# Optimization experiments

Hardware: AMD Instinct MI355X
Metric: run time of the kernel (lower is better)

The kernel has to match this reference:

```python
import jax, jax.numpy as jnp
import numpy as np

OUT, IN, SPEC = 4096, 4096, 512


def _boundprop(last_uA, weight, bias, preact_lb, preact_ub, alpha):
    # simplex_coefficient: relu(W + b[:,None]) - relu(b[:,None]), shape [OUT, IN]
    simplex_coeff = jax.nn.relu(weight + bias[:, None]) - jax.nn.relu(bias[:, None])
    pos_uA = jnp.maximum(last_uA, 0.0)  # [1, SPEC, OUT]
    neg_uA = jnpum if False else jnp.minimum(last_uA, 0.0)

    # ---- simplex branch ----
    lb_u = preact_lb[..., None]  # [1, OUT, 1]
    ub_u = preact_ub[..., None]
    upper_coeff = jnp.where(ub_u <= 0, 0.0, jnp.where(lb_u >= 0, weight, simplex_coeff))  # [1,OUT,IN]
    upper_bias = jnp.where(preact_ub <= 0, 0.0,
                           jnp.where(preact_lb >= 0, bias, jnp.maximum(bias, 0.0)))  # [1,OUT]
    lower_d = (jnp.abs(preact_lb) >= jnp.abs(preact_ub)).astype(last_uA.dtype)  # [1,OUT]
    lower_coeff = jnp.where(ub_u <= 0, 0.0,
                            jnp.where(lb_u >= 0, weight, lower_d[..., None] * weight))  # [1,OUT,IN]
    lower_bias = jnp.where(preact_ub <= 0, 0.0,
                           jnp.where(preact_lb >= 0, bias, lower_d * bias))  # [1,OUT]
    one_minus_a = 1.0 - alpha              # [1,OUT,1]
    one_minus_a_s = 1.0 - alpha[..., 0]    # [1,OUT]
    upper_coeff = one_minus_a * upper_coeff
    lower_coeff = one_minus_a * lower_coeff
    upper_bias = one_minus_a_s * upper_bias
    lower_bias = one_minus_a_s * lower_bias
    simplex_uA = (jnp.einsum('bso,boi->bsi', pos_uA, upper_coeff)
                  + jnp.einsum('bso,boi->bsi', neg_uA, lower_coeff))  # [1,SPEC,IN]
    simplex_ubias = (jnp.einsum('bso,o->bs', pos_uA, upper_bias[0])
                     + jnp.einsum('bso,o->bs', neg_uA, lower_bias[0]))  # [1,SPEC]

    # ---- crown branch ----
    lb_r = jnp.minimum(preact_lb, 0.0)
    ub_r = jnp.maximum(preact_ub, 0.0)
    ub_r = jnp.maximum(ub_r, lb_r + 1e-8)
    upper_d = ub_r / (ub_r - lb_r)  # [1,OUT]
    upper_b = -lb_r * upper_d       # [1,OUT]
    ud = upper_d[:, None, :]        # [1,1,OUT]
    ld = (ud > 0.5).astype(last_uA.dtype)
    crown_uA_pre = ud * pos_uA + ld * neg_uA  # [1,SPEC,OUT]
    crown_ubias = jnp.einsum('bso,bo->bs', pos_uA, upper_b)  # [1,SPEC]
    w = alpha * weight              # [1,OUT,IN]
    b = alpha[..., 0] * bias        # [1,OUT]
    crown_uA = jnp.einsum('bso,boi->bsi', crown_uA_pre, w)   # [1,SPEC,IN]
    crown_ubias = crown_ubias + jnp.einsum('bso,o->bs', crown_uA_pre, b[0])

    return simplex_uA + crown_uA, simplex_ubias + crown_ubias


def setup_inputs() -> dict:
    key = jax.random.key(0)
    k1, k2, k3, k4, k5 = jax.random.split(key, 5)
    weight = jax.random.normal(k1, (OUT, IN), jnp.float32) * 0.02
    bias = jax.random.normal(k2, (OUT,), jnp.float32) * 0.02
    preact_lb = jax.random.normal(k3, (1, OUT), jnp.float32)
    # ensure ub > lb, with mixed-sign ranges so all relaxation branches are hit
    preact_ub = preact_lb + jnp.abs(jax.random.normal(k4, (1, OUT), jnp.float32)) + 1e-2
    last_uA = jax.random.normal(k5, (1, SPEC, OUT), jnp.float32)
    alpha = jnp.ones((1, OUT, 1), jnp.float32)
    return {'last_uA': last_uA, 'weight': weight, 'bias': bias,
            'preact_lb': preact_lb, 'preact_ub': preact_ub, 'alpha': alpha}


def reference(last_uA, weight, bias, preact_lb, preact_ub, alpha):
    uA, ubias = _boundprop(last_uA, weight, bias, preact_lb, preact_ub, alpha)
    return uA, ubias
```

## Files before the change

### kernel.cpp

```cpp
#include <hip/hip_runtime.h>
#include <hip/hip_bf16.h>
#include <stdint.h>

#define OUTN 4096
#define INN  4096
#define SPECN 512
#define BK 128
#define KT (OUTN / BK)

typedef __attribute__((ext_vector_type(8))) short short8;
typedef __attribute__((ext_vector_type(4))) float f32x4;

__device__ __forceinline__ ushort f2bf(float f) {
    uint32_t u = __float_as_uint(f);
    uint32_t r = (u + 0x7FFFu + ((u >> 16) & 1u)) >> 16;
    return (ushort)r;
}
__device__ __forceinline__ float bf2f(ushort u) {
    return __uint_as_float((uint32_t)u << 16);
}

__global__ __launch_bounds__(256) void prep(
    const float* __restrict__ uA, const float* __restrict__ W,
    const float* __restrict__ Bias, const float* __restrict__ Lb,
    const float* __restrict__ Ub, const float* __restrict__ Alpha,
    ushort* __restrict__ A1, ushort* __restrict__ A2, ushort* __restrict__ WT,
    unsigned long long* __restrict__ rowmask, float* __restrict__ ubias_out)
{
    const int tid = threadIdx.x;
    if (blockIdx.x < 512) {
        const int s = blockIdx.x;
        float acc = 0.f;
        unsigned long long msk = 0;
        for (int p = 0; p < 4; ++p) {
            const int o = p * 1024 + tid * 4;
            const float4 u4 = *(const float4*)&uA[(size_t)s * OUTN + o];
            const float4 lb4 = *(const float4*)&Lb[o];
            const float4 ub4 = *(const float4*)&Ub[o];
            const float4 b4 = *(const float4*)&Bias[o];
            const float4 a4 = *(const float4*)&Alpha[o];
            const float uu[4] = {u4.x, u4.y, u4.z, u4.w};
            const float lbv[4] = {lb4.x, lb4.y, lb4.z, lb4.w};
            const float ubv[4] = {ub4.x, ub4.y, ub4.z, ub4.w};
            const float bv[4] = {b4.x, b4.y, b4.z, b4.w};
            const float av[4] = {a4.x, a4.y, a4.z, a4.w};
            ushort r1[4], r2[4];
#pragma unroll
            for (int j = 0; j < 4; ++j) {
                const float u = uu[j], lb = lbv[j], ub = ubv[j], b = bv[j], a = av[j];
                const float pp = fmaxf(u, 0.f), nn = fminf(u, 0.f);
                const bool stneg = (ub <= 0.f);
                const bool stpos = (lb >= 0.f);
                const float lower_d = (fabsf(lb) >= fabsf(ub)) ? 1.f : 0.f;
                float lbr = fminf(lb, 0.f);
                float ubr = fmaxf(ub, 0.f);
                ubr = fmaxf(ubr, lbr + 1e-8f);
                const float ud = ubr / (ubr - lbr);
                const float upb = -lbr * ud;
                const float ldc = (ud > 0.5f) ? 1.f : 0.f;
                const float oma = 1.f - a;
                const float crown = ud * pp + ldc * nn;
                const float wcoef = a * crown +
                    oma * (stneg ? 0.f : (stpos ? (pp + nn) : lower_d * nn));
                const float scoef = (stneg || stpos) ? 0.f : oma * pp;
                const float ub_t = stneg ? 0.f : (stpos ? b : fmaxf(b, 0.f));
                const float lb_t = stneg ? 0.f : (stpos ? b : lower_d * b);
                acc += pp * (oma * ub_t + upb) + nn * (oma * lb_t) + crown * (a * b);
                r1[j] = f2bf(wcoef);
                r2[j] = f2bf(scoef);
            }
            *(ushort4*)&A1[(size_t)s * OUTN + o] = make_ushort4(r1[0], r1[1], r1[2], r1[3]);
            *(ushort4*)&A2[(size_t)s * OUTN + o] = make_ushort4(r2[0], r2[1], r2[2], r2[3]);
            if (((r2[0] | r2[1] | r2[2] | r2[3]) & 0x7FFF) != 0)
                msk |= 1ull << (p * 16 + (tid >> 4));
        }
#pragma unroll
        for (int off = 32; off; off >>= 1) {
            acc += __shfl_down(acc, off);
            msk |= __shfl_down(msk, off);
        }
        __shared__ float redf[4];
        __shared__ unsigned long long redm[4];
        if ((tid & 63) == 0) { redf[tid >> 6] = acc; redm[tid >> 6] = msk; }
        __syncthreads();
        if (tid == 0) {
            ubias_out[s] = redf[0] + redf[1] + redf[2] + redf[3];
            rowmask[s] = redm[0] | redm[1] | redm[2] | redm[3];
        }
    } else {
        __shared__ float t[64][65];
        const int tb = blockIdx.x - 512;
        const int bi = tb & 63, bo = tb >> 6;
        const int i0 = bi * 64, o0 = bo * 64;
        const int sub = tid >> 4;
        const int q4 = (tid & 15) * 4;
#pragma unroll
        for (int p = 0; p < 4; ++p) {
            const int ol = p * 16 + sub;
            const float4 w = *(const float4*)&W[(size_t)(o0 + ol) * INN + i0 + q4];
            t[q4 + 0][ol] = w.x;
            t[q4 + 1][ol] = w.y;
            t[q4 + 2][ol] = w.z;
            t[q4 + 3][ol] = w.w;
        }
        __syncthreads();
#pragma unroll
        for (int p = 0; p < 4; ++p) {
            const int il = p * 16 + sub;
            *(ushort4*)&WT[(size_t)(i0 + il) * OUTN + o0 + q4] =
                make_ushort4(f2bf(t[il][q4]), f2bf(t[il][q4 + 1]),
                             f2bf(t[il][q4 + 2]), f2bf(t[il][q4 + 3]));
        }
    }
}

__global__ __launch_bounds__(256) void gemm(
    const ushort* __restrict__ A1, const ushort* __restrict__ A2,
    const ushort* __restrict__ WT, const float* __restrict__ Bias,
    const unsigned long long* __restrict__ rowmask, float* __restrict__ outp)
{
    __shared__ ushort sA[2][64 * BK];
    __shared__ ushort sB[2][64 * BK];
    __shared__ unsigned long long smaskLds;

    const int bid = blockIdx.x;
    const int swz = (bid & 7) * 64 + (bid >> 3);
    const int bx = swz >> 3;
    const int by = swz & 7;
    const int i0 = bx * 64, s0 = by * 64;
    const int tid = threadIdx.x;
    const int lane = tid & 63;
    const int w = tid >> 6;
    const int wr = w >> 1, wc = w & 1;

    if (tid < 64) {
        unsigned long long v = rowmask[s0 + tid];
#pragma unroll
        for (int off = 32; off; off >>= 1) v |= __shfl_down(v, off);
        if (tid == 0) smaskLds = v;
    }

    f32x4 acc[2][2] = {};

    auto stage = [&](int buf, int t) {
        const int ko = t * BK;
#pragma unroll
        for (int h = 0; h < 4; ++h) {
            const int c = w * 4 + h;
            const int r = c * 4 + (lane >> 4);
            const int g = (lane & 15) ^ (r & 15);
            const size_t off = (size_t)ko + g * 8;
            __builtin_amdgcn_global_load_lds(
                (const __attribute__((address_space(1))) void*)(A1 + (size_t)(s0 + r) * OUTN + off),
                (__attribute__((address_space(3))) void*)&sA[buf][c * 512], 16, 0, 0);
            __builtin_amdgcn_global_load_lds(
                (const __attribute__((address_space(1))) void*)(WT + (size_t)(i0 + r) * OUTN + off),
                (__attribute__((address_space(3))) void*)&sB[buf][c * 512], 16, 0, 0);
        }
    };

    auto compute = [&](int buf) {
#pragma unroll
        for (int kk = 0; kk < BK; kk += 32) {
            short8 av[2], bv[2];
#pragma unroll
            for (int m = 0; m < 2; ++m) {
                const int r = wr * 32 + m * 16 + (lane & 15);
                const int g = ((kk >> 3) + (lane >> 4)) ^ (r & 15);
                av[m] = *(const short8*)&sA[buf][r * BK + g * 8];
            }
#pragma unroll
            for (int n = 0; n < 2; ++n) {
                const int r = wc * 32 + n * 16 + (lane & 15);
                const int g = ((kk >> 3) + (lane >> 4)) ^ (r & 15);
                bv[n] = *(const short8*)&sB[buf][r * BK + g * 8];
            }
#pragma unroll
            for (int m = 0; m < 2; ++m)
#pragma unroll
                for (int n = 0; n < 2; ++n)
                    acc[m][n] = __builtin_amdgcn_mfma_f32_16x16x32_bf16(
                        av[m], bv[n], acc[m][n], 0, 0, 0);
        }
    };

    stage(0, 0);
    __syncthreads();
    const unsigned long long smask = smaskLds;
    for (int t = 0; t < KT - 1; ++t) {
        stage((t + 1) & 1, t + 1);
        compute(t & 1);
        __syncthreads();
    }
    compute((KT - 1) & 1);

    if (smask) {
        for (int b = 0; b < 64; ++b) {
            if (!((smask >> b) & 1)) continue;
            __syncthreads();
#pragma unroll
            for (int h = 0; h < 2; ++h) {
                const int c = w * 2 + h;
                const int r = c * 8 + (lane >> 3);
                const int g = (lane & 7) ^ (r & 7);
                const size_t off = (size_t)b * 64 + g * 8;
                __builtin_amdgcn_global_load_lds(
                    (const __attribute__((address_space(1))) void*)(A2 + (size_t)(s0 + r) * OUTN + off),
                    (__attribute__((address_space(3))) void*)&sA[0][c * 512], 16, 0, 0);
                __builtin_amdgcn_global_load_lds(
                    (const __attribute__((address_space(1))) void*)(WT + (size_t)(i0 + r) * OUTN + off),
                    (__attribute__((address_space(3))) void*)&sB[0][c * 512], 16, 0, 0);
            }
            __syncthreads();
#pragma unroll
            for (int kk = 0; kk < 64; kk += 32) {
                short8 av2[2], bw[2];
#pragma unroll
                for (int m = 0; m < 2; ++m) {
                    const int r = wr * 32 + m * 16 + (lane & 15);
                    const int g = ((kk >> 3) + (lane >> 4)) ^ (r & 7);
                    av2[m] = *(const short8*)&sA[0][r * 64 + g * 8];
                }
                const int kb = kk + (lane >> 4) * 8;
                const float4 b0 = *(const float4*)&Bias[b * 64 + kb];
                const float4 b1 = *(const float4*)&Bias[b * 64 + kb + 4];
                const float bb[8] = {b0.x, b0.y, b0.z, b0.w, b1.x, b1.y, b1.z, b1.w};
#pragma unroll
                for (int n = 0; n < 2; ++n) {
                    const int r = wc * 32 + n * 16 + (lane & 15);
                    const int g = ((kk >> 3) + (lane >> 4)) ^ (r & 7);
                    const short8 wv = *(const short8*)&sB[0][r * 64 + g * 8];
                    short8 sv;
#pragma unroll
                    for (int j = 0; j < 8; ++j) {
                        const float wf = bf2f((ushort)wv[j]);
                        sv[j] = (short)f2bf(fmaxf(wf + bb[j], 0.f) - fmaxf(bb[j], 0.f));
                    }
                    bw[n] = sv;
                }
#pragma unroll
                for (int m = 0; m < 2; ++m)
#pragma unroll
                    for (int n = 0; n < 2; ++n)
                        acc[m][n] = __builtin_amdgcn_mfma_f32_16x16x32_bf16(
                            av2[m], bw[n], acc[m][n], 0, 0, 0);
            }
        }
    }

#pragma unroll
    for (int m = 0; m < 2; ++m)
#pragma unroll
        for (int n = 0; n < 2; ++n) {
            const int srow = s0 + wr * 32 + m * 16 + (lane >> 4) * 4;
            const int icol = i0 + wc * 32 + n * 16 + (lane & 15);
#pragma unroll
            for (int r = 0; r < 4; ++r)
                outp[(size_t)(srow + r) * INN + icol] = acc[m][n][r];
        }
}

extern "C" void kernel_launch(void* const* d_in, const int* in_sizes, int n_in,
                              void* d_out, int out_size, void* d_ws, size_t ws_size,
                              hipStream_t stream) {
    const float* uA    = (const float*)d_in[0];
    const float* W     = (const float*)d_in[1];
    const float* Bias  = (const float*)d_in[2];
    const float* Lb    = (const float*)d_in[3];
    const float* Ub    = (const float*)d_in[4];
    const float* Alpha = (const float*)d_in[5];
    float* outp = (float*)d_out;

    char* ws = (char*)d_ws;
    unsigned long long* rowmask = (unsigned long long*)ws;
    ushort* A1 = (ushort*)(ws + 4096);
    ushort* A2 = (ushort*)(ws + 4096 + (1u << 22));
    ushort* WT = (ushort*)(ws + 4096 + (2u << 22));

    prep<<<4608, 256, 0, stream>>>(uA, W, Bias, Lb, Ub, Alpha, A1, A2, WT,
                                   rowmask, outp + (size_t)SPECN * INN);
    gemm<<<512, 256, 0, stream>>>(A1, A2, WT, Bias, rowmask, outp);
}
```

Measured before the change: 146.6 us.

## Triple-buffer GEMM K-loop with BK 64 and a single barrier per step

Shrinks the K tile from 128 to 64 and moves from double to triple buffering in LDS. Each iteration waits on vmcnt for the older stage and then issues one raw s_barrier, so two stages of loads stay in flight while the block computes. The row-mask reduction now uses a per-wave xor shuffle instead of an LDS round-trip and the extra barrier. The tail loop reuses the stage lambda, which issues redundant A1 loads that are then overwritten by A2 loads into the same LDS slots. That adds some extra traffic and relies on the in-order completion of the two sets of writes.

```diff
diff --git a/kernel.cpp b/kernel.cpp
--- a/kernel.cpp
+++ b/kernel.cpp
@@ -5,7 +5,7 @@
 #define OUTN 4096
 #define INN  4096
 #define SPECN 512
-#define BK 128
+#define BK 64
 #define KT (OUTN / BK)
 
 typedef __attribute__((ext_vector_type(8))) short short8;
@@ -119,9 +119,8 @@
     const ushort* __restrict__ WT, const float* __restrict__ Bias,
     const unsigned long long* __restrict__ rowmask, float* __restrict__ outp)
 {
-    __shared__ ushort sA[2][64 * BK];
-    __shared__ ushort sB[2][64 * BK];
-    __shared__ unsigned long long smaskLds;
+    __shared__ ushort sA[3][64 * 64];
+    __shared__ ushort sB[3][64 * 64];
 
     const int bid = blockIdx.x;
     const int swz = (bid & 7) * 64 + (bid >> 3);
@@ -133,30 +132,30 @@
     const int w = tid >> 6;
     const int wr = w >> 1, wc = w & 1;
 
-    if (tid < 64) {
-        unsigned long long v = rowmask[s0 + tid];
-#pragma unroll
-        for (int off = 32; off; off >>= 1) v |= __shfl_down(v, off);
-        if (tid == 0) smaskLds = v;
-    }
+    unsigned long long smask = rowmask[s0 + lane];
+#pragma unroll
+    for (int off = 32; off; off >>= 1) smask |= __shfl_xor(smask, off);
 
     f32x4 acc[2][2] = {};
+
+    const int c0 = w * 2, c1 = w * 2 + 1;
+    const int rr0 = c0 * 8 + (lane >> 3), rr1 = c1 * 8 + (lane >> 3);
+    const int g0 = (lane & 7) ^ (rr0 & 7), g1 = (lane & 7) ^ (rr1 & 7);
 
     auto stage = [&](int buf, int t) {
         const int ko = t * BK;
-#pragma unroll
-        for (int h = 0; h < 4; ++h) {
-            const int c = w * 4 + h;
-            const int r = c * 4 + (lane >> 4);
-            const int g = (lane & 15) ^ (r & 15);
-            const size_t off = (size_t)ko + g * 8;
-            __builtin_amdgcn_global_load_lds(
-                (const __attribute__((address_space(1))) void*)(A1 + (size_t)(s0 + r) * OUTN + off),
-                (__attribute__((address_space(3))) void*)&sA[buf][c * 512], 16, 0, 0);
-            __builtin_amdgcn_global_load_lds(
-                (const __attribute__((address_space(1))) void*)(WT + (size_t)(i0 + r) * OUTN + off),
-                (__attribute__((address_space(3))) void*)&sB[buf][c * 512], 16, 0, 0);
-        }
+        __builtin_amdgcn_global_load_lds(
+            (const __attribute__((address_space(1))) void*)(A1 + (size_t)(s0 + rr0) * OUTN + ko + g0 * 8),
+            (__attribute__((address_space(3))) void*)&sA[buf][c0 * 512], 16, 0, 0);
+        __builtin_amdgcn_global_load_lds(
+            (const __attribute__((address_space(1))) void*)(A1 + (size_t)(s0 + rr1) * OUTN + ko + g1 * 8),
+            (__attribute__((address_space(3))) void*)&sA[buf][c1 * 512], 16, 0, 0);
+        __builtin_amdgcn_global_load_lds(
+            (const __attribute__((address_space(1))) void*)(WT + (size_t)(i0 + rr0) * OUTN + ko + g0 * 8),
+            (__attribute__((address_space(3))) void*)&sB[buf][c0 * 512], 16, 0, 0);
+        __builtin_amdgcn_global_load_lds(
+            (const __attribute__((address_space(1))) void*)(WT + (size_t)(i0 + rr1) * OUTN + ko + g1 * 8),
+            (__attribute__((address_space(3))) void*)&sB[buf][c1 * 512], 16, 0, 0);
     };
 
     auto compute = [&](int buf) {
@@ -166,14 +165,14 @@
 #pragma unroll
             for (int m = 0; m < 2; ++m) {
                 const int r = wr * 32 + m * 16 + (lane & 15);
-                const int g = ((kk >> 3) + (lane >> 4)) ^ (r & 15);
-                av[m] = *(const short8*)&sA[buf][r * BK + g * 8];
+                const int g = ((kk >> 3) + (lane >> 4)) ^ (r & 7);
+                av[m] = *(const short8*)&sA[buf][r * 64 + g * 8];
             }
 #pragma unroll
             for (int n = 0; n < 2; ++n) {
                 const int r = wc * 32 + n * 16 + (lane & 15);
-                const int g = ((kk >> 3) + (lane >> 4)) ^ (r & 15);
-                bv[n] = *(const short8*)&sB[buf][r * BK + g * 8];
+                const int g = ((kk >> 3) + (lane >> 4)) ^ (r & 7);
+                bv[n] = *(const short8*)&sB[buf][r * 64 + g * 8];
             }
 #pragma unroll
             for (int m = 0; m < 2; ++m)
@@ -185,32 +184,30 @@
     };
 
     stage(0, 0);
-    __syncthreads();
-    const unsigned long long smask = smaskLds;
+    stage(1, 1);
     for (int t = 0; t < KT - 1; ++t) {
-        stage((t + 1) & 1, t + 1);
-        compute(t & 1);
-        __syncthreads();
+        asm volatile("s_waitcnt vmcnt(4)" ::: "memory");
+        __builtin_amdgcn_sched_barrier(0);
+        __builtin_amdgcn_s_barrier();
+        if (t + 2 < KT) stage((t + 2) % 3, t + 2);
+        compute(t % 3);
     }
-    compute((KT - 1) & 1);
+    asm volatile("s_waitcnt vmcnt(0)" ::: "memory");
+    __builtin_amdgcn_sched_barrier(0);
+    __builtin_amdgcn_s_barrier();
+    compute((KT - 1) % 3);
 
     if (smask) {
         for (int b = 0; b < 64; ++b) {
             if (!((smask >> b) & 1)) continue;
             __syncthreads();
-#pragma unroll
-            for (int h = 0; h < 2; ++h) {
-                const int c = w * 2 + h;
-                const int r = c * 8 + (lane >> 3);
-                const int g = (lane & 7) ^ (r & 7);
-                const size_t off = (size_t)b * 64 + g * 8;
-                __builtin_amdgcn_global_load_lds(
-                    (const __attribute__((address_space(1))) void*)(A2 + (size_t)(s0 + r) * OUTN + off),
-                    (__attribute__((address_space(3))) void*)&sA[0][c * 512], 16, 0, 0);
-                __builtin_amdgcn_global_load_lds(
-                    (const __attribute__((address_space(1))) void*)(WT + (size_t)(i0 + r) * OUTN + off),
-                    (__attribute__((address_space(3))) void*)&sB[0][c * 512], 16, 0, 0);
-            }
+            stage(0, b);
+            __builtin_amdgcn_global_load_lds(
+                (const __attribute__((address_space(1))) void*)(A2 + (size_t)(s0 + rr0) * OUTN + b * 64 + g0 * 8),
+                (__attribute__((address_space(3))) void*)&sA[0][c0 * 512], 16, 0, 0);
+            __builtin_amdgcn_global_load_lds(
+                (const __attribute__((address_space(1))) void*)(A2 + (size_t)(s0 + rr1) * OUTN + b * 64 + g1 * 8),
+                (__attribute__((address_space(3))) void*)&sA[0][c1 * 512], 16, 0, 0);
             __syncthreads();
 #pragma unroll
             for (int kk = 0; kk < 64; kk += 32) {
```

After: 158.0 us. +7.7%, slower.

## Split K across waves in GEMM with LDS reduction of partial tiles

Applied to the files above, without the earlier changes.

Replaces the 2x2 wave tiling of the 64x64 output tile with an intra-block split-K: each of the four waves computes the full 64x64 tile over its own 32-wide K slice of every BK chunk, and the partial accumulators are then summed through shared memory before the store. The intent is to halve LDS fragment reads per MFMA, since each wave now reuses 4 A and 4 B fragments across 16 MFMAs. In exchange, each wave holds 64 accumulator registers, which may lower occupancy, and an LDS reduction is added at the end. In the sparse simplex correction pass only two waves do work.

```diff
diff --git a/kernel.cpp b/kernel.cpp
--- a/kernel.cpp
+++ b/kernel.cpp
@@ -119,9 +119,7 @@
     const ushort* __restrict__ WT, const float* __restrict__ Bias,
     const unsigned long long* __restrict__ rowmask, float* __restrict__ outp)
 {
-    __shared__ ushort sA[2][64 * BK];
-    __shared__ ushort sB[2][64 * BK];
-    __shared__ unsigned long long smaskLds;
+    __shared__ __align__(16) ushort smem[2][2][64 * BK];
 
     const int bid = blockIdx.x;
     const int swz = (bid & 7) * 64 + (bid >> 3);
@@ -131,62 +129,52 @@
     const int tid = threadIdx.x;
     const int lane = tid & 63;
     const int w = tid >> 6;
-    const int wr = w >> 1, wc = w & 1;
-
-    if (tid < 64) {
-        unsigned long long v = rowmask[s0 + tid];
-#pragma unroll
-        for (int off = 32; off; off >>= 1) v |= __shfl_down(v, off);
-        if (tid == 0) smaskLds = v;
-    }
-
-    f32x4 acc[2][2] = {};
+
+    unsigned long long smask = rowmask[s0 + lane];
+#pragma unroll
+    for (int off = 32; off; off >>= 1) smask |= __shfl_xor(smask, off);
+
+    f32x4 acc[4][4] = {};
 
     auto stage = [&](int buf, int t) {
         const int ko = t * BK;
 #pragma unroll
         for (int h = 0; h < 4; ++h) {
             const int c = w * 4 + h;
-            const int r = c * 4 + (lane >> 4);
-            const int g = (lane & 15) ^ (r & 15);
-            const size_t off = (size_t)ko + g * 8;
+            const int row = c * 4 + (lane >> 4);
+            const int g = (lane & 15) ^ (row & 15);
             __builtin_amdgcn_global_load_lds(
-                (const __attribute__((address_space(1))) void*)(A1 + (size_t)(s0 + r) * OUTN + off),
-                (__attribute__((address_space(3))) void*)&sA[buf][c * 512], 16, 0, 0);
+                (const __attribute__((address_space(1))) void*)(A1 + (size_t)(s0 + row) * OUTN + ko + g * 8),
+                (__attribute__((address_space(3))) void*)&smem[0][buf][c * 512], 16, 0, 0);
             __builtin_amdgcn_global_load_lds(
-                (const __attribute__((address_space(1))) void*)(WT + (size_t)(i0 + r) * OUTN + off),
-                (__attribute__((address_space(3))) void*)&sB[buf][c * 512], 16, 0, 0);
+                (const __attribute__((address_space(1))) void*)(WT + (size_t)(i0 + row) * OUTN + ko + g * 8),
+                (__attribute__((address_space(3))) void*)&smem[1][buf][c * 512], 16, 0, 0);
         }
     };
 
     auto compute = [&](int buf) {
-#pragma unroll
-        for (int kk = 0; kk < BK; kk += 32) {
-            short8 av[2], bv[2];
-#pragma unroll
-            for (int m = 0; m < 2; ++m) {
-                const int r = wr * 32 + m * 16 + (lane & 15);
-                const int g = ((kk >> 3) + (lane >> 4)) ^ (r & 15);
-                av[m] = *(const short8*)&sA[buf][r * BK + g * 8];
-            }
-#pragma unroll
-            for (int n = 0; n < 2; ++n) {
-                const int r = wc * 32 + n * 16 + (lane & 15);
-                const int g = ((kk >> 3) + (lane >> 4)) ^ (r & 15);
-                bv[n] = *(const short8*)&sB[buf][r * BK + g * 8];
-            }
-#pragma unroll
-            for (int m = 0; m < 2; ++m)
-#pragma unroll
-                for (int n = 0; n < 2; ++n)
-                    acc[m][n] = __builtin_amdgcn_mfma_f32_16x16x32_bf16(
-                        av[m], bv[n], acc[m][n], 0, 0, 0);
-        }
+        const int kc = w * 4 + (lane >> 4);
+        short8 av[4], bv[4];
+#pragma unroll
+        for (int m = 0; m < 4; ++m) {
+            const int r = m * 16 + (lane & 15);
+            av[m] = *(const short8*)&smem[0][buf][r * BK + (kc ^ (r & 15)) * 8];
+        }
+#pragma unroll
+        for (int n = 0; n < 4; ++n) {
+            const int r = n * 16 + (lane & 15);
+            bv[n] = *(const short8*)&smem[1][buf][r * BK + (kc ^ (r & 15)) * 8];
+        }
+#pragma unroll
+        for (int m = 0; m < 4; ++m)
+#pragma unroll
+            for (int n = 0; n < 4; ++n)
+                acc[m][n] = __builtin_amdgcn_mfma_f32_16x16x32_bf16(
+                    av[m], bv[n], acc[m][n], 0, 0, 0);
     };
 
     stage(0, 0);
     __syncthreads();
-    const unsigned long long smask = smaskLds;
     for (int t = 0; t < KT - 1; ++t) {
         stage((t + 1) & 1, t + 1);
         compute(t & 1);
@@ -201,35 +189,33 @@
 #pragma unroll
             for (int h = 0; h < 2; ++h) {
                 const int c = w * 2 + h;
-                const int r = c * 8 + (lane >> 3);
-                const int g = (lane & 7) ^ (r & 7);
-                const size_t off = (size_t)b * 64 + g * 8;
+                const int row = c * 8 + (lane >> 3);
+                const int g = (lane & 7) ^ (row & 7);
                 __builtin_amdgcn_global_load_lds(
-                    (const __attribute__((address_space(1))) void*)(A2 + (size_t)(s0 + r) * OUTN + off),
-                    (__attribute__((address_space(3))) void*)&sA[0][c * 512], 16, 0, 0);
+                    (const __attribute__((address_space(1))) void*)(A2 + (size_t)(s0 + row) * OUTN + b * 64 + g * 8),
+                    (__attribute__((address_space(3))) void*)&smem[0][0][c * 512], 16, 0, 0);
                 __builtin_amdgcn_global_load_lds(
-                    (const __attribute__((address_space(1))) void*)(WT + (size_t)(i0 + r) * OUTN + off),
-                    (__attribute__((address_space(3))) void*)&sB[0][c * 512], 16, 0, 0);
+                    (const __attribute__((address_space(1))) void*)(WT + (size_t)(i0 + row) * OUTN + b * 64 + g * 8),
+                    (__attribute__((address_space(3))) void*)&smem[1][0][c * 512], 16, 0, 0);
             }
             __syncthreads();
-#pragma unroll
-            for (int kk = 0; kk < 64; kk += 32) {
-                short8 av2[2], bw[2];
-#pragma unroll
-                for (int m = 0; m < 2; ++m) {
-                    const int r = wr * 32 + m * 16 + (lane & 15);
-                    const int g = ((kk >> 3) + (lane >> 4)) ^ (r & 7);
-                    av2[m] = *(const short8*)&sA[0][r * 64 + g * 8];
+            if (w < 2) {
+                const int kk = w * 32;
+                const int kc8 = (kk >> 3) + (lane >> 4);
+                short8 av2[4], bw[4];
+#pragma unroll
+                for (int m = 0; m < 4; ++m) {
+                    const int r = m * 16 + (lane & 15);
+                    av2[m] = *(const short8*)&smem[0][0][r * 64 + (kc8 ^ (r & 7)) * 8];
                 }
                 const int kb = kk + (lane >> 4) * 8;
                 const float4 b0 = *(const float4*)&Bias[b * 64 + kb];
                 const float4 b1 = *(const float4*)&Bias[b * 64 + kb + 4];
                 const float bb[8] = {b0.x, b0.y, b0.z, b0.w, b1.x, b1.y, b1.z, b1.w};
 #pragma unroll
-                for (int n = 0; n < 2; ++n) {
-                    const int r = wc * 32 + n * 16 + (lane & 15);
-                    const int g = ((kk >> 3) + (lane >> 4)) ^ (r & 7);
-                    const short8 wv = *(const short8*)&sB[0][r * 64 + g * 8];
+                for (int n = 0; n < 4; ++n) {
+                    const int r = n * 16 + (lane & 15);
+                    const short8 wv = *(const short8*)&smem[1][0][r * 64 + (kc8 ^ (r & 7)) * 8];
                     short8 sv;
 #pragma unroll
                     for (int j = 0; j < 8; ++j) {
@@ -239,25 +225,38 @@
                     bw[n] = sv;
                 }
 #pragma unroll
-                for (int m = 0; m < 2; ++m)
-#pragma unroll
-                    for (int n = 0; n < 2; ++n)
+                for (int m = 0; m < 4; ++m)
+#pragma unroll
+                    for (int n = 0; n < 4; ++n)
                         acc[m][n] = __builtin_amdgcn_mfma_f32_16x16x32_bf16(
                             av2[m], bw[n], acc[m][n], 0, 0, 0);
             }
         }
     }
 
-#pragma unroll
-    for (int m = 0; m < 2; ++m)
-#pragma unroll
-        for (int n = 0; n < 2; ++n) {
-            const int srow = s0 + wr * 32 + m * 16 + (lane >> 4) * 4;
-            const int icol = i0 + wc * 32 + n * 16 + (lane & 15);
-#pragma unroll
-            for (int r = 0; r < 4; ++r)
-                outp[(size_t)(srow + r) * INN + icol] = acc[m][n][r];
-        }
+    __syncthreads();
+    float* facc = (float*)smem;
+#pragma unroll
+    for (int m = 0; m < 4; ++m)
+#pragma unroll
+        for (int n = 0; n < 4; ++n)
+            *(f32x4*)&facc[w * 4096 + (m * 4 + n) * 256 + lane * 4] = acc[m][n];
+    __syncthreads();
+#pragma unroll
+    for (int n = 0; n < 4; ++n) {
+        f32x4 s = *(const f32x4*)&facc[(w * 4 + n) * 256 + lane * 4];
+#pragma unroll
+        for (int wp = 1; wp < 4; ++wp) {
+            const f32x4 v = *(const f32x4*)&facc[wp * 4096 + (w * 4 + n) * 256 + lane * 4];
+            s.x += v.x; s.y += v.y; s.z += v.z; s.w += v.w;
+        }
+        const int srow = s0 + w * 16 + (lane >> 4) * 4;
+        const int icol = i0 + n * 16 + (lane & 15);
+        outp[(size_t)(srow + 0) * INN + icol] = s.x;
+        outp[(size_t)(srow + 1) * INN + icol] = s.y;
+        outp[(size_t)(srow + 2) * INN + icol] = s.z;
+        outp[(size_t)(srow + 3) * INN + icol] = s.w;
+    }
 }
 
 extern "C" void kernel_launch(void* const* d_in, const int* in_sizes, int n_in,
```

Measured after the change: 145.5 us. Within noise of the previous version (-0.8%).
